# Performance work log

Measured on AMD Instinct MI355X. Metric: run time of the kernel, lower is better.

The kernel has to match this reference:

```python
import jax, jax.numpy as jnp
import numpy as np

H, L, NB = 128, 2048, 64  # features, seq len, half state size (conj-symmetric N=128)


def _forward(u, x_re, x_im, Lambda_re, Lambda_im, B_re, B_im, C_re, C_im, D, d):
    Lam = (Lambda_re + 1j * Lambda_im).astype(jnp.complex64)   # (H, NB) discrete diag A
    B = (B_re + 1j * B_im).astype(jnp.complex64)               # (H, NB)
    C = (C_re + 1j * C_im).astype(jnp.complex64)               # (H, NB)
    x0 = (x_re + 1j * x_im).astype(jnp.complex64)              # (H, NB) initial state
    Hn, Ln = u.shape
    # scan elements (A_t, b_t, d_t); identity element (1, x0, False) prepended at t=0
    A = jnp.concatenate([jnp.ones((Hn, 1, NB), jnp.complex64),
                         jnp.broadcast_to(Lam[:, None, :], (Hn, Ln, NB))], axis=1)
    b = jnp.concatenate([x0[:, None, :],
                         B[:, None, :] * u[:, :, None].astype(jnp.complex64)], axis=1)
    dd = jnp.concatenate([jnp.zeros((1,), bool), d.astype(bool)])[None, :, None]  # (1, L+1, 1)

    def combine(lhs, rhs):
        # reset-aware associative combine: if right done-flag set, drop left contribution
        A_i, b_i, c_i = lhs
        A_j, b_j, c_j = rhs
        return (jnp.where(c_j, A_j, A_j * A_i),
                jnp.where(c_j, b_j, A_j * b_i + b_j),
                jnp.logical_or(c_i, c_j))

    _, xs, _ = jax.lax.associative_scan(combine, (A, b, dd), axis=1)
    xs = xs[:, 1:]                                             # (H, L, NB) hidden states
    # conj symmetry: y_t = 2*Re(C @ x_t) + D * u_t
    y = 2.0 * jnp.real(jnp.einsum('hn,hln->hl', C, xs)) + D[:, None] * u
    return y, xs[:, -1]


def setup_inputs():
    key = jax.random.key(0)
    ks = jax.random.split(key, 8)
    # stable ZOH-discretized HiPPO-like diagonal system (mirrors LSSL-f init)
    dts = jnp.logspace(-3.0, -1.0, H)                          # (H,) per-feature timescales
    k = jnp.arange(NB, dtype=jnp.float32)
    lam_c = -0.5 + 1j * jnp.pi * (2.0 * k + 1.0)               # (NB,) continuous poles
    lam_d = jnp.exp(dts[:, None] * lam_c[None, :]).astype(jnp.complex64)  # (H, NB), |.|<1
    Bc = ((jax.random.normal(ks[0], (NB,)) + 1j * jax.random.normal(ks[1], (NB,)))
          / jnp.sqrt(2.0 * NB)).astype(jnp.complex64)
    Bd = (((lam_d - 1.0) / lam_c[None, :]) * Bc[None, :]).astype(jnp.complex64)  # (H, NB)
    C = ((jax.random.normal(ks[2], (H, NB)) + 1j * jax.random.normal(ks[3], (H, NB)))
         / jnp.sqrt(float(NB))).astype(jnp.complex64)
    return {
        "u": jax.random.normal(ks[4], (H, L), jnp.float32),
        "x_re": jnp.zeros((H, NB), jnp.float32),
        "x_im": jnp.zeros((H, NB), jnp.float32),
        "Lambda_re": jnp.real(lam_d).astype(jnp.float32),
        "Lambda_im": jnp.imag(lam_d).astype(jnp.float32),
        "B_re": jnp.real(Bd).astype(jnp.float32),
        "B_im": jnp.imag(Bd).astype(jnp.float32),
        "C_re": jnp.real(C).astype(jnp.float32),
        "C_im": jnp.imag(C).astype(jnp.float32),
        "D": jax.random.normal(ks[5], (H,), jnp.float32),
        "d": jax.random.bernoulli(ks[6], 0.01, (L,)),
    }


def reference(u, x_re, x_im, Lambda_re, Lambda_im, B_re, B_im, C_re, C_im, D, d):
    return _forward(u, x_re, x_im, Lambda_re, Lambda_im, B_re, B_im, C_re, C_im, D, d)
```

## Files before the change

### kernel.cpp

```cpp
#include <hip/hip_runtime.h>

#define Hn 128
#define Ln 2048
#define NBn 64
#define K 64
#define G 32
#define PITCH 65


__global__ __launch_bounds__(64) void phase1_local(
    const float* __restrict__ u,
    const float* __restrict__ Lre,  const float* __restrict__ Lim,
    const float* __restrict__ Bre,  const float* __restrict__ Bim,
    const float* __restrict__ Cre,  const float* __restrict__ Cim,
    const float* __restrict__ Dv,   const int* __restrict__ dflag,
    float* __restrict__ out,
    float4* __restrict__ Sum)
{
    __shared__ float g_s[K * PITCH];
    __shared__ float u_s[K];

    const int g = blockIdx.x, h = blockIdx.y, n = threadIdx.x;
    const int hn = h * NBn + n;
    const int l0 = g * K;

    const float lre = Lre[hn], lim = Lim[hn];
    const float br  = Bre[hn], bi  = Bim[hn];
    const float cr  = Cre[hn], ci  = Cim[hn];
    const float Dh  = Dv[h];
    const float cbr2 = 2.f * (cr * br - ci * bi);
    const float cbi2 = 2.f * (cr * bi + ci * br);

    u_s[n] = u[h * Ln + l0 + n];
    const unsigned long long m = __ballot(dflag[l0 + n] != 0);
    __syncthreads();

    float wr = 0.f, wi = 0.f;
    if (m == 0ull) {
        #pragma unroll
        for (int k = 0; k < K; ++k) {
            const float uk = u_s[k];
            const float nr = fmaf(lre, wr, fmaf(-lim, wi, cbr2 * uk));
            const float ni = fmaf(lre, wi, fmaf( lim, wr, cbi2 * uk));
            wr = nr; wi = ni;
            g_s[k * PITCH + n] = wr;
        }
    } else {
        #pragma unroll
        for (int k = 0; k < K; ++k) {
            const bool  rs  = (m >> k) & 1ull;
            const float lrk = rs ? 0.f : lre;
            const float lik = rs ? 0.f : lim;
            const float uk  = u_s[k];
            const float nr = fmaf(lrk, wr, fmaf(-lik, wi, cbr2 * uk));
            const float ni = fmaf(lrk, wi, fmaf( lik, wr, cbi2 * uk));
            wr = nr; wi = ni;
            g_s[k * PITCH + n] = wr;
        }
    }
    __syncthreads();

    const float* row = g_s + n * PITCH;
    float a0 = 0.f, a1 = 0.f, a2 = 0.f, a3 = 0.f;
    #pragma unroll
    for (int k = 0; k < NBn; k += 4) {
        a0 += row[k + 0]; a1 += row[k + 1];
        a2 += row[k + 2]; a3 += row[k + 3];
    }
    out[h * Ln + l0 + n] = (a0 + a1) + (a2 + a3) + Dh * u_s[n];

    float pr = lre, pi = lim;
    #pragma unroll
    for (int it = 0; it < 6; ++it) {
        const float sr2 = pr * pr - pi * pi;
        const float si2 = 2.f * pr * pi;
        pr = sr2; pi = si2;
    }
    if (m) { pr = 0.f; pi = 0.f; }
    Sum[(h * G + g) * NBn + n] = make_float4(pr, pi, wr, wi);
}

__global__ __launch_bounds__(64) void phase23_fixup(
    const float* __restrict__ x_re, const float* __restrict__ x_im,
    const float* __restrict__ Lre,  const float* __restrict__ Lim,
    const float* __restrict__ Cre,  const float* __restrict__ Cim,
    const int* __restrict__ dflag,
    const float4* __restrict__ Sum,
    float* __restrict__ out)
{
    __shared__ float g_s[K * PITCH];

    const int g = blockIdx.x, h = blockIdx.y, n = threadIdx.x;
    const int hn = h * NBn + n;
    const int l0 = g * K;

    const float cr = Cre[hn], ci = Cim[hn];
    const float x0r = x_re[hn], x0i = x_im[hn];
    float sre = 2.f * (cr * x0r - ci * x0i);
    float sim = 2.f * (cr * x0i + ci * x0r);

    const float4* base = Sum + h * G * NBn + n;
    #pragma unroll
    for (int j = 0; j < G; ++j) {
        const float4 s = base[j * NBn];
        if (j < g) {
            const float nr = fmaf(s.x, sre, fmaf(-s.y, sim, s.z));
            const float ni = fmaf(s.x, sim, fmaf( s.y, sre, s.w));
            sre = nr; sim = ni;
        }
    }

    if (g == G - 1) {
        const float4 s = base[(G - 1) * NBn];
        const float fr = fmaf(s.x, sre, fmaf(-s.y, sim, s.z));
        const float fi = fmaf(s.x, sim, fmaf( s.y, sre, s.w));
        const float c2r = 2.f * cr, c2i = 2.f * ci;
        const float inv = 1.f / (c2r * c2r + c2i * c2i);
        float* xlast = out + Hn * Ln;
        xlast[2 * hn + 0] = (fr * c2r + fi * c2i) * inv;
        xlast[2 * hn + 1] = (fi * c2r - fr * c2i) * inv;
    }

    const float lre = Lre[hn], lim = Lim[hn];
    const unsigned long long bal = __ballot(dflag[l0 + n] != 0);
    const int kr = bal ? (__ffsll((long long)bal) - 1) : K;

    const float l2r = lre * lre - lim * lim;
    const float l2i = 2.f * lre * lim;

    float tAr = fmaf(lre, sre, -lim * sim);
    float tAi = fmaf(lre, sim,  lim * sre);
    float tBr = fmaf(l2r, sre, -l2i * sim);
    float tBi = fmaf(l2r, sim,  l2i * sre);
    g_s[0 * PITCH + n] = tAr;
    g_s[1 * PITCH + n] = tBr;
    #pragma unroll
    for (int k = 2; k < K; k += 2) {
        const float nAr = fmaf(l2r, tAr, -l2i * tAi);
        const float nAi = fmaf(l2r, tAi,  l2i * tAr);
        tAr = nAr; tAi = nAi;
        g_s[k * PITCH + n] = tAr;
        const float nBr = fmaf(l2r, tBr, -l2i * tBi);
        const float nBi = fmaf(l2r, tBi,  l2i * tBr);
        tBr = nBr; tBi = nBi;
        g_s[(k + 1) * PITCH + n] = tBr;
    }
    __syncthreads();

    const float* row = g_s + n * PITCH;
    float a0 = 0.f, a1 = 0.f, a2 = 0.f, a3 = 0.f;
    #pragma unroll
    for (int k = 0; k < NBn; k += 4) {
        a0 += row[k + 0]; a1 += row[k + 1];
        a2 += row[k + 2]; a3 += row[k + 3];
    }
    if (n < kr)
        out[h * Ln + l0 + n] += (a0 + a1) + (a2 + a3);
}

extern "C" void kernel_launch(void* const* d_in, const int* in_sizes, int n_in,
                              void* d_out, int out_size, void* d_ws, size_t ws_size,
                              hipStream_t stream) {
    const float* u    = (const float*)d_in[0];
    const float* x_re = (const float*)d_in[1];
    const float* x_im = (const float*)d_in[2];
    const float* Lre  = (const float*)d_in[3];
    const float* Lim  = (const float*)d_in[4];
    const float* Bre  = (const float*)d_in[5];
    const float* Bim  = (const float*)d_in[6];
    const float* Cre  = (const float*)d_in[7];
    const float* Cim  = (const float*)d_in[8];
    const float* Dv   = (const float*)d_in[9];
    const int*   dfl  = (const int*)d_in[10];
    float* out = (float*)d_out;

    float4* Sum = (float4*)d_ws;

    dim3 grid(G, Hn);
    phase1_local<<<grid, 64, 0, stream>>>(u, Lre, Lim, Bre, Bim, Cre, Cim,
                                          Dv, dfl, out, Sum);
    phase23_fixup<<<grid, 64, 0, stream>>>(x_re, x_im, Lre, Lim, Cre, Cim,
                                           dfl, Sum, out);
}
```

Measured before the change: 107.2 us.

## Restructure fixup kernel to one block per feature with sequential carry

The second kernel moves from a (G, H) grid of 64-thread blocks, where each block redundantly re-scans all preceding chunk summaries, to one 256-thread block per feature. Each block stages that feature's chunk summaries in shared memory and walks the carry sequentially, and its four waves take turns doing the per-chunk state-correction work. This removes the quadratic redundant carry propagation and the repeated global reads of Sum. In exchange there are only 128 blocks, so parallelism is lower, and every wave still runs the full serial carry loop over all 32 chunks.

```diff
diff --git a/kernel.cpp b/kernel.cpp
--- a/kernel.cpp
+++ b/kernel.cpp
@@ -8,7 +8,7 @@
 #define PITCH 65
 
 
-__global__ __launch_bounds__(64) void phase1_local(
+__global__ __launch_bounds__(64) void phaseA_local(
     const float* __restrict__ u,
     const float* __restrict__ Lre,  const float* __restrict__ Lim,
     const float* __restrict__ Bre,  const float* __restrict__ Bim,
@@ -80,7 +80,7 @@
     Sum[(h * G + g) * NBn + n] = make_float4(pr, pi, wr, wi);
 }
 
-__global__ __launch_bounds__(64) void phase23_fixup(
+__global__ __launch_bounds__(256) void phaseB_head(
     const float* __restrict__ x_re, const float* __restrict__ x_im,
     const float* __restrict__ Lre,  const float* __restrict__ Lim,
     const float* __restrict__ Cre,  const float* __restrict__ Cim,
@@ -88,74 +88,82 @@
     const float4* __restrict__ Sum,
     float* __restrict__ out)
 {
-    __shared__ float g_s[K * PITCH];
+    __shared__ float4 S_s[G * NBn];
+    __shared__ float  g_s[4][K * PITCH];
 
-    const int g = blockIdx.x, h = blockIdx.y, n = threadIdx.x;
+    const int h = blockIdx.x, tid = threadIdx.x;
+    const int w = tid >> 6, n = tid & 63;
     const int hn = h * NBn + n;
-    const int l0 = g * K;
 
-    const float cr = Cre[hn], ci = Cim[hn];
+    const float4* src = Sum + h * G * NBn;
+    #pragma unroll
+    for (int i = 0; i < 8; ++i)
+        S_s[tid + 256 * i] = src[tid + 256 * i];
+
+    unsigned long long mk[8];
+    #pragma unroll
+    for (int jj = 0; jj < 8; ++jj)
+        mk[jj] = __ballot(dflag[(4 * jj + w) * K + n] != 0);
+
+    const float lre = Lre[hn], lim = Lim[hn];
+    const float cr  = Cre[hn], ci  = Cim[hn];
     const float x0r = x_re[hn], x0i = x_im[hn];
     float sre = 2.f * (cr * x0r - ci * x0i);
     float sim = 2.f * (cr * x0i + ci * x0r);
+    const float l2r = lre * lre - lim * lim;
+    const float l2i = 2.f * lre * lim;
 
-    const float4* base = Sum + h * G * NBn + n;
+    __syncthreads();
+
+    float* gbuf = g_s[w];
     #pragma unroll
     for (int j = 0; j < G; ++j) {
-        const float4 s = base[j * NBn];
-        if (j < g) {
-            const float nr = fmaf(s.x, sre, fmaf(-s.y, sim, s.z));
-            const float ni = fmaf(s.x, sim, fmaf( s.y, sre, s.w));
-            sre = nr; sim = ni;
+        if ((j & 3) == w) {
+            const int jj = j >> 2;
+            const int l0 = j * K;
+            const unsigned long long mm = mk[jj];
+            const int kr = mm ? (__ffsll((long long)mm) - 1) : K;
+
+            float tAr = fmaf(lre, sre, -lim * sim);
+            float tAi = fmaf(lre, sim,  lim * sre);
+            float tBr = fmaf(l2r, sre, -l2i * sim);
+            float tBi = fmaf(l2r, sim,  l2i * sre);
+            gbuf[0 * PITCH + n] = tAr;
+            gbuf[1 * PITCH + n] = tBr;
+            #pragma unroll
+            for (int k = 2; k < K; k += 2) {
+                const float nAr = fmaf(l2r, tAr, -l2i * tAi);
+                const float nAi = fmaf(l2r, tAi,  l2i * tAr);
+                tAr = nAr; tAi = nAi;
+                gbuf[k * PITCH + n] = tAr;
+                const float nBr = fmaf(l2r, tBr, -l2i * tBi);
+                const float nBi = fmaf(l2r, tBi,  l2i * tBr);
+                tBr = nBr; tBi = nBi;
+                gbuf[(k + 1) * PITCH + n] = tBr;
+            }
+            const float* row = gbuf + n * PITCH;
+            float a0 = 0.f, a1 = 0.f, a2 = 0.f, a3 = 0.f;
+            #pragma unroll
+            for (int k = 0; k < NBn; k += 4) {
+                a0 += row[k + 0]; a1 += row[k + 1];
+                a2 += row[k + 2]; a3 += row[k + 3];
+            }
+            if (n < kr)
+                out[h * Ln + l0 + n] += (a0 + a1) + (a2 + a3);
         }
+        const float4 s = S_s[j * NBn + n];
+        const float nr = fmaf(s.x, sre, fmaf(-s.y, sim, s.z));
+        const float ni = fmaf(s.x, sim, fmaf( s.y, sre, s.w));
+        sre = nr; sim = ni;
     }
 
-    if (g == G - 1) {
-        const float4 s = base[(G - 1) * NBn];
-        const float fr = fmaf(s.x, sre, fmaf(-s.y, sim, s.z));
-        const float fi = fmaf(s.x, sim, fmaf( s.y, sre, s.w));
+    if (w == 0) {
         const float c2r = 2.f * cr, c2i = 2.f * ci;
         const float inv = 1.f / (c2r * c2r + c2i * c2i);
         float* xlast = out + Hn * Ln;
-        xlast[2 * hn + 0] = (fr * c2r + fi * c2i) * inv;
-        xlast[2 * hn + 1] = (fi * c2r - fr * c2i) * inv;
+        xlast[2 * hn + 0] = (sre * c2r + sim * c2i) * inv;
+        xlast[2 * hn + 1] = (sim * c2r - sre * c2i) * inv;
     }
-
-    const float lre = Lre[hn], lim = Lim[hn];
-    const unsigned long long bal = __ballot(dflag[l0 + n] != 0);
-    const int kr = bal ? (__ffsll((long long)bal) - 1) : K;
-
-    const float l2r = lre * lre - lim * lim;
-    const float l2i = 2.f * lre * lim;
-
-    float tAr = fmaf(lre, sre, -lim * sim);
-    float tAi = fmaf(lre, sim,  lim * sre);
-    float tBr = fmaf(l2r, sre, -l2i * sim);
-    float tBi = fmaf(l2r, sim,  l2i * sre);
-    g_s[0 * PITCH + n] = tAr;
-    g_s[1 * PITCH + n] = tBr;
-    #pragma unroll
-    for (int k = 2; k < K; k += 2) {
-        const float nAr = fmaf(l2r, tAr, -l2i * tAi);
-        const float nAi = fmaf(l2r, tAi,  l2i * tAr);
-        tAr = nAr; tAi = nAi;
-        g_s[k * PITCH + n] = tAr;
-        const float nBr = fmaf(l2r, tBr, -l2i * tBi);
-        const float nBi = fmaf(l2r, tBi,  l2i * tBr);
-        tBr = nBr; tBi = nBi;
-        g_s[(k + 1) * PITCH + n] = tBr;
-    }
-    __syncthreads();
-
-    const float* row = g_s + n * PITCH;
-    float a0 = 0.f, a1 = 0.f, a2 = 0.f, a3 = 0.f;
-    #pragma unroll
-    for (int k = 0; k < NBn; k += 4) {
-        a0 += row[k + 0]; a1 += row[k + 1];
-        a2 += row[k + 2]; a3 += row[k + 3];
-    }
-    if (n < kr)
-        out[h * Ln + l0 + n] += (a0 + a1) + (a2 + a3);
 }
 
 extern "C" void kernel_launch(void* const* d_in, const int* in_sizes, int n_in,
@@ -176,9 +184,9 @@
 
     float4* Sum = (float4*)d_ws;
 
-    dim3 grid(G, Hn);
-    phase1_local<<<grid, 64, 0, stream>>>(u, Lre, Lim, Bre, Bim, Cre, Cim,
-                                          Dv, dfl, out, Sum);
-    phase23_fixup<<<grid, 64, 0, stream>>>(x_re, x_im, Lre, Lim, Cre, Cim,
-                                           dfl, Sum, out);
+    dim3 gridA(G, Hn);
+    phaseA_local<<<gridA, 64, 0, stream>>>(u, Lre, Lim, Bre, Bim, Cre, Cim,
+                                           Dv, dfl, out, Sum);
+    phaseB_head<<<Hn, 256, 0, stream>>>(x_re, x_im, Lre, Lim, Cre, Cim,
+                                        dfl, Sum, out);
 }
```

After: 96.61 us. 1.11x faster.
